# Performance work log

Measured on AMD Instinct MI355X. Metric: run time of the kernel, lower is better.

The kernel has to match this reference:

```python
import jax, jax.numpy as jnp
import numpy as np

HARMONICS = 5


def _harmonic_basis(x):
    k = jnp.arange(1, HARMONICS + 1, dtype=x.dtype)            # [H]
    kx = x[..., None] * k                                       # [B, D, H]
    sc = jnp.stack([jnp.sin(kx), jnp.cos(kx)], axis=-1)         # [B, D, H, 2]
    sc = sc.reshape(*x.shape, 2 * HARMONICS)                    # interleaved sin/cos
    ones = jnp.ones((*x.shape, 1), dtype=x.dtype)
    return jnp.concatenate([ones, sc], axis=-1)                 # [B, D, 2H+1]


def setup_inputs() -> dict:
    key = jax.random.key(0)
    k1, k2, k3 = jax.random.split(key, 3)
    B, D, F, H = 16384, 256, 11, 256
    x = jax.random.normal(k1, (B, D), dtype=jnp.float32)
    W = jax.random.normal(k2, (D, F, H), dtype=jnp.float32) * (1.0 / np.sqrt(F))
    b = jax.random.normal(k3, (D, H), dtype=jnp.float32) * 0.01
    return {"x": x, "W": W, "b": b}


def reference(x, W, b) -> jnp.ndarray:
    # basis expansion per feature, batched small GEMM, summed over features
    basis = _harmonic_basis(x)                                  # [B, D, F]
    out = jnp.einsum('bdf,dfh->bh', basis, W)                   # sum over features fused
    out = out + jnp.sum(b, axis=0)                              # sum of per-feature biases
    return out
```

## Files before the change

### kernel.cpp

```cpp
#include <hip/hip_runtime.h>
#include <hip/hip_bf16.h>


#define BDIM 16384
#define DDIM 256
#define HOUT 256
#define KTOT 2560
#define NKT  80
#define BM 64
#define BN 128
#define LDA_S 328

typedef __bf16 bf16x8 __attribute__((ext_vector_type(8)));
typedef float floatx4 __attribute__((ext_vector_type(4)));

__device__ __forceinline__ unsigned short f2bf(float f) {
    unsigned int u = __float_as_uint(f);
    return (unsigned short)((u + 0x7FFFu + ((u >> 16) & 1u)) >> 16);
}

__device__ __forceinline__ unsigned int pkbf(float a, float b) {
    __hip_bfloat162 r = __float22bfloat162_rn(make_float2(a, b));
    return *reinterpret_cast<unsigned int*>(&r);
}

__global__ void prep_kernel(const float* __restrict__ W, const float* __restrict__ bias,
                            unsigned short* __restrict__ Wfrag, float* __restrict__ c_part) {
    const int bid = blockIdx.x;
    const int t = threadIdx.x;
    if (bid < NKT) {
        const int kt = bid;
        const int dtile = kt / 10;
        const int f = kt - dtile * 10 + 1;
        const float* wsrc = W + ((size_t)(dtile * 32) * 11 + f) * 256 + t;
        union { unsigned short s[32]; int4 v[4]; } buf;
#pragma unroll
        for (int dd = 0; dd < 32; ++dd)
            buf.s[dd] = f2bf(wsrc[(size_t)dd * 11 * 256]);
        int4* dst = (int4*)(Wfrag + ((size_t)kt * 256 + t) * 32);
#pragma unroll
        for (int v = 0; v < 4; ++v) dst[v] = buf.v[v];
    } else {
        const int p = bid - NKT;
        float acc = 0.f;
#pragma unroll
        for (int dd = 0; dd < 32; ++dd) {
            const int d = p * 32 + dd;
            acc += W[(size_t)(d * 11) * 256 + t] + bias[(size_t)d * 256 + t];
        }
        c_part[p * 256 + t] = acc;
    }
}

__global__ __launch_bounds__(256, 2)
void kan_gemm(const float* __restrict__ x, const unsigned short* __restrict__ Wfrag,
              const float* __restrict__ c_part, float* __restrict__ out) {
    __shared__ unsigned short As[BM * LDA_S];

    const int t = threadIdx.x;
    const int m0 = blockIdx.x * BM;
    const int h0 = blockIdx.y * BN;

    const int lane = t & 63;
    const int wave = t >> 6;
    const int wr = wave >> 1;
    const int wc = wave & 1;
    const int l15 = lane & 15;
    const int koff = lane >> 4;

    const int m_a = lane;
    const int q = wave;

    floatx4 acc[2][4];
#pragma unroll
    for (int i = 0; i < 2; ++i)
#pragma unroll
        for (int j = 0; j < 4; ++j)
            acc[i][j] = (floatx4){0.f, 0.f, 0.f, 0.f};

    const float* xrow = x + (size_t)(m0 + m_a) * DDIM;
    const unsigned short* bbase = Wfrag + (size_t)(h0 + wc * 64 + l15) * 32 + koff * 8;

    float4 xa = *(const float4*)(xrow + q * 8);
    float4 xb = *(const float4*)(xrow + q * 8 + 4);

    for (int dtile = 0; dtile < 8; ++dtile) {
        float xv[8] = {xa.x, xa.y, xa.z, xa.w, xb.x, xb.y, xb.z, xb.w};

        union { unsigned int u[4]; int4 v; } av[10];
#pragma unroll
        for (int p = 0; p < 4; ++p) {
            float sa, ca, sb, cb;
            __sincosf(xv[2 * p],     &sa, &ca);
            __sincosf(xv[2 * p + 1], &sb, &cb);
            float ska = sa, cka = ca, skb = sb, ckb = cb;
            av[0].u[p] = pkbf(ska, skb);
            av[1].u[p] = pkbf(cka, ckb);
#pragma unroll
            for (int k = 2; k <= 5; ++k) {
                const float nsa = ska * ca + cka * sa;
                const float nca = cka * ca - ska * sa;
                const float nsb = skb * cb + ckb * sb;
                const float ncb = ckb * cb - skb * sb;
                ska = nsa; cka = nca; skb = nsb; ckb = ncb;
                av[2 * k - 2].u[p] = pkbf(ska, skb);
                av[2 * k - 1].u[p] = pkbf(cka, ckb);
            }
        }
        unsigned short* arow = &As[m_a * LDA_S];
#pragma unroll
        for (int hs = 0; hs < 10; ++hs)
            *(int4*)(arow + hs * 32 + q * 8) = av[hs].v;

        __syncthreads();

        if (dtile < 7) {
            xa = *(const float4*)(xrow + (dtile + 1) * 32 + q * 8);
            xb = *(const float4*)(xrow + (dtile + 1) * 32 + q * 8 + 4);
        }

#pragma unroll
        for (int hs = 0; hs < 10; ++hs) {
            const int kt = dtile * 10 + hs;
            bf16x8 bfrag[4];
#pragma unroll
            for (int j = 0; j < 4; ++j)
                bfrag[j] = *(const bf16x8*)(bbase + (size_t)kt * 8192 + j * 512);
            bf16x8 afrag[2];
#pragma unroll
            for (int i = 0; i < 2; ++i)
                afrag[i] = *(const bf16x8*)(&As[(wr * 32 + i * 16 + l15) * LDA_S + hs * 32 + koff * 8]);
#pragma unroll
            for (int i = 0; i < 2; ++i)
#pragma unroll
                for (int j = 0; j < 4; ++j)
                    acc[i][j] = __builtin_amdgcn_mfma_f32_16x16x32_bf16(afrag[i], bfrag[j], acc[i][j], 0, 0, 0);
        }
        __syncthreads();
    }

    float cj[4];
#pragma unroll
    for (int j = 0; j < 4; ++j) {
        const int col = h0 + wc * 64 + j * 16 + l15;
        float s = 0.f;
#pragma unroll
        for (int p = 0; p < 8; ++p) s += c_part[p * 256 + col];
        cj[j] = s;
    }
#pragma unroll
    for (int i = 0; i < 2; ++i) {
        const int row0 = m0 + wr * 32 + i * 16 + koff * 4;
#pragma unroll
        for (int j = 0; j < 4; ++j) {
            const int col = h0 + wc * 64 + j * 16 + l15;
#pragma unroll
            for (int r = 0; r < 4; ++r)
                out[(size_t)(row0 + r) * HOUT + col] = acc[i][j][r] + cj[j];
        }
    }
}

extern "C" void kernel_launch(void* const* d_in, const int* in_sizes, int n_in,
                              void* d_out, int out_size, void* d_ws, size_t ws_size,
                              hipStream_t stream) {
    const float* x = (const float*)d_in[0];
    const float* W = (const float*)d_in[1];
    const float* b = (const float*)d_in[2];
    float* out = (float*)d_out;

    unsigned short* Wfrag = (unsigned short*)d_ws;
    float* c_part = (float*)((char*)d_ws + (size_t)NKT * 256 * 32 * 2);

    prep_kernel<<<NKT + 8, 256, 0, stream>>>(W, b, Wfrag, c_part);
    kan_gemm<<<dim3(BDIM / BM, HOUT / BN), 256, 0, stream>>>(x, Wfrag, c_part, out);
}
```

Baseline: 120.3 us.

## Store A tile in MFMA fragment layout, Chebyshev harmonics, double-buffer fragment loads

The shared A tile is reorganised into a fragment-major layout, so each lane writes and reads one contiguous 16-byte chunk with no padding and no bank conflicts. Higher harmonics now come from the Chebyshev recurrence, which needs fewer multiplies than angle addition, and each harmonic is written as it is produced, which lowers register pressure. B and A fragments for the next k-slice are loaded into a second register buffer while the current MFMAs run, to hide load latency. The recurrence may accumulate slightly more error, and the extra buffers add registers.

```diff
diff --git a/kernel.cpp b/kernel.cpp
--- a/kernel.cpp
+++ b/kernel.cpp
@@ -9,7 +9,6 @@
 #define NKT  80
 #define BM 64
 #define BN 128
-#define LDA_S 328
 
 typedef __bf16 bf16x8 __attribute__((ext_vector_type(8)));
 typedef float floatx4 __attribute__((ext_vector_type(4)));
@@ -55,7 +54,7 @@
 __global__ __launch_bounds__(256, 2)
 void kan_gemm(const float* __restrict__ x, const unsigned short* __restrict__ Wfrag,
               const float* __restrict__ c_part, float* __restrict__ out) {
-    __shared__ unsigned short As[BM * LDA_S];
+    __shared__ unsigned short As[10 * 4 * 512];
 
     const int t = threadIdx.x;
     const int m0 = blockIdx.x * BM;
@@ -70,6 +69,8 @@
 
     const int m_a = lane;
     const int q = wave;
+    const int it_w = m_a >> 4;
+    const int slot = (m_a & 15) + 16 * q;
 
     floatx4 acc[2][4];
 #pragma unroll
@@ -86,32 +87,34 @@
 
     for (int dtile = 0; dtile < 8; ++dtile) {
         float xv[8] = {xa.x, xa.y, xa.z, xa.w, xb.x, xb.y, xb.z, xb.w};
-
-        union { unsigned int u[4]; int4 v; } av[10];
+        float sc[8], cc[8], sp[8], cp[8], t2c[8];
 #pragma unroll
-        for (int p = 0; p < 4; ++p) {
-            float sa, ca, sb, cb;
-            __sincosf(xv[2 * p],     &sa, &ca);
-            __sincosf(xv[2 * p + 1], &sb, &cb);
-            float ska = sa, cka = ca, skb = sb, ckb = cb;
-            av[0].u[p] = pkbf(ska, skb);
-            av[1].u[p] = pkbf(cka, ckb);
+        for (int j = 0; j < 8; ++j) {
+            __sincosf(xv[j], &sc[j], &cc[j]);
+            t2c[j] = cc[j] + cc[j];
+            sp[j] = 0.f;
+            cp[j] = 1.f;
+        }
 #pragma unroll
-            for (int k = 2; k <= 5; ++k) {
-                const float nsa = ska * ca + cka * sa;
-                const float nca = cka * ca - ska * sa;
-                const float nsb = skb * cb + ckb * sb;
-                const float ncb = ckb * cb - skb * sb;
-                ska = nsa; cka = nca; skb = nsb; ckb = ncb;
-                av[2 * k - 2].u[p] = pkbf(ska, skb);
-                av[2 * k - 1].u[p] = pkbf(cka, ckb);
+        for (int k = 1; k <= 5; ++k) {
+            union { unsigned int u[4]; int4 v; } vs, vc;
+#pragma unroll
+            for (int p = 0; p < 4; ++p) {
+                vs.u[p] = pkbf(sc[2 * p], sc[2 * p + 1]);
+                vc.u[p] = pkbf(cc[2 * p], cc[2 * p + 1]);
+            }
+            *(int4*)(&As[((2 * k - 2) * 4 + it_w) * 512 + slot * 8]) = vs.v;
+            *(int4*)(&As[((2 * k - 1) * 4 + it_w) * 512 + slot * 8]) = vc.v;
+            if (k < 5) {
+#pragma unroll
+                for (int j = 0; j < 8; ++j) {
+                    const float ns = t2c[j] * sc[j] - sp[j];
+                    const float nc = t2c[j] * cc[j] - cp[j];
+                    sp[j] = sc[j]; cp[j] = cc[j];
+                    sc[j] = ns;   cc[j] = nc;
+                }
             }
         }
-        unsigned short* arow = &As[m_a * LDA_S];
-#pragma unroll
-        for (int hs = 0; hs < 10; ++hs)
-            *(int4*)(arow + hs * 32 + q * 8) = av[hs].v;
-
         __syncthreads();
 
         if (dtile < 7) {
@@ -119,22 +122,35 @@
             xb = *(const float4*)(xrow + (dtile + 1) * 32 + q * 8 + 4);
         }
 
+        const unsigned short* bkt = bbase + (size_t)(dtile * 10) * 8192;
+
+        bf16x8 bf0[4], bf1[4], af0[2], af1[2];
+#pragma unroll
+        for (int j = 0; j < 4; ++j)
+            bf0[j] = *(const bf16x8*)(bkt + j * 512);
+#pragma unroll
+        for (int i = 0; i < 2; ++i)
+            af0[i] = *(const bf16x8*)(&As[(0 * 4 + wr * 2 + i) * 512 + lane * 8]);
+
 #pragma unroll
         for (int hs = 0; hs < 10; ++hs) {
-            const int kt = dtile * 10 + hs;
-            bf16x8 bfrag[4];
+            bf16x8* bnext = (hs & 1) ? bf0 : bf1;
+            bf16x8* anext = (hs & 1) ? af0 : af1;
+            if (hs < 9) {
 #pragma unroll
-            for (int j = 0; j < 4; ++j)
-                bfrag[j] = *(const bf16x8*)(bbase + (size_t)kt * 8192 + j * 512);
-            bf16x8 afrag[2];
+                for (int j = 0; j < 4; ++j)
+                    bnext[j] = *(const bf16x8*)(bkt + (size_t)(hs + 1) * 8192 + j * 512);
 #pragma unroll
-            for (int i = 0; i < 2; ++i)
-                afrag[i] = *(const bf16x8*)(&As[(wr * 32 + i * 16 + l15) * LDA_S + hs * 32 + koff * 8]);
+                for (int i = 0; i < 2; ++i)
+                    anext[i] = *(const bf16x8*)(&As[((hs + 1) * 4 + wr * 2 + i) * 512 + lane * 8]);
+            }
+            const bf16x8* bcur = (hs & 1) ? bf1 : bf0;
+            const bf16x8* acur = (hs & 1) ? af1 : af0;
 #pragma unroll
             for (int i = 0; i < 2; ++i)
 #pragma unroll
                 for (int j = 0; j < 4; ++j)
-                    acc[i][j] = __builtin_amdgcn_mfma_f32_16x16x32_bf16(afrag[i], bfrag[j], acc[i][j], 0, 0, 0);
+                    acc[i][j] = __builtin_amdgcn_mfma_f32_16x16x32_bf16(acur[i], bcur[j], acc[i][j], 0, 0, 0);
         }
         __syncthreads();
     }
```

Result: faster. 117.0 us (-2.7%).

## Generate harmonic A fragments in registers, drop LDS staging and barriers

Applied to the files above, without the earlier changes.

Removes the shared-memory A tile and its barriers. Each wave now computes its own bf16 basis fragments directly in registers from sin, cos and cos2x using Chebyshev-style identities. The tiling changes to 64x32 per wave, and B fragments are software-prefetched one k-step ahead. In exchange, the trig and harmonic generation is repeated across all eight column blocks, register pressure rises, and B operands get no shared reuse between waves.

```diff
diff --git a/kernel.cpp b/kernel.cpp
--- a/kernel.cpp
+++ b/kernel.cpp
@@ -2,14 +2,9 @@
 #include <hip/hip_bf16.h>
 
 
-#define BDIM 16384
+#define HOUT 256
 #define DDIM 256
-#define HOUT 256
-#define KTOT 2560
 #define NKT  80
-#define BM 64
-#define BN 128
-#define LDA_S 328
 
 typedef __bf16 bf16x8 __attribute__((ext_vector_type(8)));
 typedef float floatx4 __attribute__((ext_vector_type(4)));
@@ -22,6 +17,24 @@
 __device__ __forceinline__ unsigned int pkbf(float a, float b) {
     __hip_bfloat162 r = __float22bfloat162_rn(make_float2(a, b));
     return *reinterpret_cast<unsigned int*>(&r);
+}
+
+__device__ __forceinline__ float harm(int hs, float s1, float c1, float c2) {
+    switch (hs) {
+    case 0: return s1;
+    case 1: return c1;
+    case 2: return (s1 + s1) * c1;
+    case 3: return c2;
+    case 4: return __builtin_fmaf(c2 + c2, s1, s1);
+    case 5: return __builtin_fmaf(c2 + c2, c1, -c1);
+    case 6: return (c2 + c2) * ((s1 + s1) * c1);
+    case 7: return __builtin_fmaf(c2 + c2, c2, -1.f);
+    case 8: { const float s3 = __builtin_fmaf(c2 + c2, s1, s1);
+              return __builtin_fmaf(c2 + c2, s3, -s1); }
+    case 9: { const float c3 = __builtin_fmaf(c2 + c2, c1, -c1);
+              return __builtin_fmaf(c2 + c2, c3, -c1); }
+    }
+    return 0.f;
 }
 
 __global__ void prep_kernel(const float* __restrict__ W, const float* __restrict__ bias,
@@ -55,108 +68,112 @@
 __global__ __launch_bounds__(256, 2)
 void kan_gemm(const float* __restrict__ x, const unsigned short* __restrict__ Wfrag,
               const float* __restrict__ c_part, float* __restrict__ out) {
-    __shared__ unsigned short As[BM * LDA_S];
-
     const int t = threadIdx.x;
-    const int m0 = blockIdx.x * BM;
-    const int h0 = blockIdx.y * BN;
-
     const int lane = t & 63;
     const int wave = t >> 6;
-    const int wr = wave >> 1;
-    const int wc = wave & 1;
     const int l15 = lane & 15;
     const int koff = lane >> 4;
 
-    const int m_a = lane;
-    const int q = wave;
+    const int m0 = blockIdx.x * 256 + wave * 64;
+    const int n0 = blockIdx.y * 32;
 
-    floatx4 acc[2][4];
+    const unsigned short* bptr = Wfrag + (size_t)(n0 + l15) * 32 + koff * 8;
+
+    const float* xbase = x + (size_t)(m0 + l15) * DDIM + koff * 8;
+
+    floatx4 acc[4][2];
 #pragma unroll
-    for (int i = 0; i < 2; ++i)
+    for (int it = 0; it < 4; ++it)
 #pragma unroll
-        for (int j = 0; j < 4; ++j)
-            acc[i][j] = (floatx4){0.f, 0.f, 0.f, 0.f};
+        for (int jt = 0; jt < 2; ++jt)
+            acc[it][jt] = (floatx4){0.f, 0.f, 0.f, 0.f};
 
-    const float* xrow = x + (size_t)(m0 + m_a) * DDIM;
-    const unsigned short* bbase = Wfrag + (size_t)(h0 + wc * 64 + l15) * 32 + koff * 8;
+    float4 xq[8];
+#pragma unroll
+    for (int it = 0; it < 4; ++it) {
+        xq[2 * it]     = *(const float4*)(xbase + it * 16 * DDIM);
+        xq[2 * it + 1] = *(const float4*)(xbase + it * 16 * DDIM + 4);
+    }
 
-    float4 xa = *(const float4*)(xrow + q * 8);
-    float4 xb = *(const float4*)(xrow + q * 8 + 4);
+    bf16x8 bc[2], bn[2];
+    bc[0] = *(const bf16x8*)(bptr);
+    bc[1] = *(const bf16x8*)(bptr + 512);
+
+    float s1[4][8], c1[4][8], c2[4][8];
 
     for (int dtile = 0; dtile < 8; ++dtile) {
-        float xv[8] = {xa.x, xa.y, xa.z, xa.w, xb.x, xb.y, xb.z, xb.w};
-
-        union { unsigned int u[4]; int4 v; } av[10];
 #pragma unroll
-        for (int p = 0; p < 4; ++p) {
-            float sa, ca, sb, cb;
-            __sincosf(xv[2 * p],     &sa, &ca);
-            __sincosf(xv[2 * p + 1], &sb, &cb);
-            float ska = sa, cka = ca, skb = sb, ckb = cb;
-            av[0].u[p] = pkbf(ska, skb);
-            av[1].u[p] = pkbf(cka, ckb);
+        for (int it = 0; it < 4; ++it) {
+            const float xs[8] = {xq[2 * it].x, xq[2 * it].y, xq[2 * it].z, xq[2 * it].w,
+                                 xq[2 * it + 1].x, xq[2 * it + 1].y, xq[2 * it + 1].z, xq[2 * it + 1].w};
 #pragma unroll
-            for (int k = 2; k <= 5; ++k) {
-                const float nsa = ska * ca + cka * sa;
-                const float nca = cka * ca - ska * sa;
-                const float nsb = skb * cb + ckb * sb;
-                const float ncb = ckb * cb - skb * sb;
-                ska = nsa; cka = nca; skb = nsb; ckb = ncb;
-                av[2 * k - 2].u[p] = pkbf(ska, skb);
-                av[2 * k - 1].u[p] = pkbf(cka, ckb);
+            for (int jj = 0; jj < 8; ++jj) {
+                float s, c;
+                __sincosf(xs[jj], &s, &c);
+                s1[it][jj] = s;
+                c1[it][jj] = c;
+                c2[it][jj] = __builtin_fmaf(c + c, c, -1.f);
             }
         }
-        unsigned short* arow = &As[m_a * LDA_S];
-#pragma unroll
-        for (int hs = 0; hs < 10; ++hs)
-            *(int4*)(arow + hs * 32 + q * 8) = av[hs].v;
-
-        __syncthreads();
 
         if (dtile < 7) {
-            xa = *(const float4*)(xrow + (dtile + 1) * 32 + q * 8);
-            xb = *(const float4*)(xrow + (dtile + 1) * 32 + q * 8 + 4);
+            const float* xn = xbase + (dtile + 1) * 32;
+#pragma unroll
+            for (int it = 0; it < 4; ++it) {
+                xq[2 * it]     = *(const float4*)(xn + it * 16 * DDIM);
+                xq[2 * it + 1] = *(const float4*)(xn + it * 16 * DDIM + 4);
+            }
         }
+
+        const unsigned short* bkt = bptr + (size_t)dtile * 10 * 8192;
 
 #pragma unroll
         for (int hs = 0; hs < 10; ++hs) {
-            const int kt = dtile * 10 + hs;
-            bf16x8 bfrag[4];
+            bn[0] = *(const bf16x8*)(bkt + (size_t)(hs + 1) * 8192);
+            bn[1] = *(const bf16x8*)(bkt + (size_t)(hs + 1) * 8192 + 512);
+
+            bf16x8 af[4];
 #pragma unroll
-            for (int j = 0; j < 4; ++j)
-                bfrag[j] = *(const bf16x8*)(bbase + (size_t)kt * 8192 + j * 512);
-            bf16x8 afrag[2];
+            for (int it = 0; it < 4; ++it) {
+                union { unsigned int u[4]; bf16x8 v; } a;
 #pragma unroll
-            for (int i = 0; i < 2; ++i)
-                afrag[i] = *(const bf16x8*)(&As[(wr * 32 + i * 16 + l15) * LDA_S + hs * 32 + koff * 8]);
+                for (int p = 0; p < 4; ++p) {
+                    const float va = harm(hs, s1[it][2 * p], c1[it][2 * p], c2[it][2 * p]);
+                    const float vb = harm(hs, s1[it][2 * p + 1], c1[it][2 * p + 1], c2[it][2 * p + 1]);
+                    a.u[p] = pkbf(va, vb);
+                }
+                af[it] = a.v;
+            }
+
 #pragma unroll
-            for (int i = 0; i < 2; ++i)
+            for (int it = 0; it < 4; ++it)
 #pragma unroll
-                for (int j = 0; j < 4; ++j)
-                    acc[i][j] = __builtin_amdgcn_mfma_f32_16x16x32_bf16(afrag[i], bfrag[j], acc[i][j], 0, 0, 0);
+                for (int jt = 0; jt < 2; ++jt)
+                    acc[it][jt] = __builtin_amdgcn_mfma_f32_16x16x32_bf16(af[it], bc[jt], acc[it][jt], 0, 0, 0);
+
+            bc[0] = bn[0];
+            bc[1] = bn[1];
         }
-        __syncthreads();
     }
 
-    float cj[4];
+    float cj[2];
 #pragma unroll
-    for (int j = 0; j < 4; ++j) {
-        const int col = h0 + wc * 64 + j * 16 + l15;
+    for (int jt = 0; jt < 2; ++jt) {
+        const int col = n0 + jt * 16 + l15;
         float s = 0.f;
 #pragma unroll
         for (int p = 0; p < 8; ++p) s += c_part[p * 256 + col];
-        cj[j] = s;
+        cj[jt] = s;
     }
 #pragma unroll
-    for (int i = 0; i < 2; ++i) {
-        const int row0 = m0 + wr * 32 + i * 16 + koff * 4;
+    for (int it = 0; it < 4; ++it) {
+        const int row0 = m0 + it * 16 + koff * 4;
 #pragma unroll
-        for (int j = 0; j < 4; ++j) {
-            const int col = h0 + wc * 64 + j * 16 + l15;
+        for (int jt = 0; jt < 2; ++jt) {
+            const int col = n0 + jt * 16 + l15;
 #pragma unroll
             for (int r = 0; r < 4; ++r)
-                out[(size_t)(row0 + r) * HOUT + col] = acc[i][j][r] + cj[j];
+                out[(size_t)(row0 + r) * HOUT + col] = acc[it][jt][r] + cj[jt];
         }
     }
 }
@@ -173,5 +190,5 @@
     float* c_part = (float*)((char*)d_ws + (size_t)NKT * 256 * 32 * 2);
 
     prep_kernel<<<NKT + 8, 256, 0, stream>>>(W, b, Wfrag, c_part);
-    kan_gemm<<<dim3(BDIM / BM, HOUT / BN), 256, 0, stream>>>(x, Wfrag, c_part, out);
+    kan_gemm<<<dim3(64, 8), 256, 0, stream>>>(x, Wfrag, c_part, out);
 }
```

Result: slower. 141.0 us (+17.3%).
